# Optimization experiments

Hardware: AMD Instinct MI355X
Metric: run time of the kernel (lower is better)

Reference implementation:

```python
import jax, jax.numpy as jnp
import numpy as np

V = 6          # num_variables
K = 6          # codebook_size
D = 32         # embedding_dim
C = 3          # channels
B = 64         # batch
N = K ** V     # 46656 codebook combinations
EPS = 1e-5     # torch BatchNorm eps
ENTROPY_SCALE = 0.1


def setup_inputs() -> dict:
    key = jax.random.key(0)
    ks = jax.random.split(key, 40)
    i = iter(range(40))
    def rn(shape, s):
        return jax.random.normal(ks[next(i)], shape, dtype=jnp.float32) * s
    def rv(shape):
        return 0.5 + 0.5 * jax.random.uniform(ks[next(i)], shape, dtype=jnp.float32)
    inp = {
        'x': jax.random.normal(ks[next(i)], (B, C, 7, 7), dtype=jnp.float32),
        # encoder
        'conv_w': rn((256, C, 7, 7), 0.08), 'conv_b': rn((256,), 0.01),
        'ebn2_g': 1.0 + rn((256,), 0.1), 'ebn2_b': rn((256,), 0.1),
        'fc1_w': rn((1024, 256), 0.06), 'fc1_b': rn((1024,), 0.01),
        'ebn1_g': 1.0 + rn((1024,), 0.1), 'ebn1_b': rn((1024,), 0.1),
        'fc2_w': rn((V * K, 1024), 0.03), 'fc2_b': rn((V * K,), 0.01),
        # quantizer embeddings (V separate codebooks)
        'embeds': jax.random.normal(ks[next(i)], (V, K, D), dtype=jnp.float32),
        # decoder
        'dfc1_w': rn((1024, V * D), 0.07), 'dfc1_b': rn((1024,), 0.01),
        'dbn1_g': 1.0 + rn((1024,), 0.1), 'dbn1_b': rn((1024,), 0.1),
        'dbn1_rm': rn((1024,), 0.1), 'dbn1_rv': rv((1024,)),
        'dfc2_w': rn((256, 1024), 0.03), 'dfc2_b': rn((256,), 0.01),
        'dbn2_g': 1.0 + rn((256,), 0.1), 'dbn2_b': rn((256,), 0.1),
        'dbn2_rm': rn((256,), 0.1), 'dbn2_rv': rv((256,)),
        'dct1_w': rn((256, 16, 7, 7), 0.05), 'dct1_b': rn((16,), 0.01),
        'dbn3_g': 1.0 + rn((16,), 0.1), 'dbn3_b': rn((16,), 0.1),
        'dbn3_rm': rn((16,), 0.1), 'dbn3_rv': rv((16,)),
        'dct2_w': rn((16, C), 0.2), 'dct2_b': rn((C,), 0.01),
    }
    return inp


def _bn_eval(t, g, b, rm, rvar):
    # eval-mode BatchNorm (running stats); params broadcast over leading dims
    return g * (t - rm) * jax.lax.rsqrt(rvar + EPS) + b


def _bn_train(t, g, b):
    # train-mode BatchNorm1d on (B, F): biased batch statistics over dim 0
    m = t.mean(0)
    v = ((t - m) ** 2).mean(0)
    return g * (t - m) * jax.lax.rsqrt(v + EPS) + b


def _decode_all(embeds, dfc1_w, dfc1_b, dbn1_g, dbn1_b, dbn1_rm, dbn1_rv,
                dfc2_w, dfc2_b, dbn2_g, dbn2_b, dbn2_rm, dbn2_rv,
                dct1_w, dct1_b, dbn3_g, dbn3_b, dbn3_rm, dbn3_rv,
                dct2_w, dct2_b):
    # enumerate all K^V index tuples in itertools.product order (first var slowest)
    idx = jnp.arange(N)
    powers = K ** (V - 1 - jnp.arange(V))
    combos = (idx[:, None] // powers[None, :]) % K          # (N, V)
    z = embeds[jnp.arange(V)[None, :], combos]              # (N, V, D) gather
    h = z.reshape(N, V * D) @ dfc1_w.T + dfc1_b             # (N, 1024)
    h = jax.nn.relu(_bn_eval(h, dbn1_g, dbn1_b, dbn1_rm, dbn1_rv))
    h = h @ dfc2_w.T + dfc2_b                               # (N, 256)
    h = jax.nn.relu(_bn_eval(h, dbn2_g, dbn2_b, dbn2_rm, dbn2_rv))
    # ConvTranspose2d(256,16,7,stride=2) on 1x1 input == einsum with full kernel
    h = jnp.einsum('ni,iohw->nohw', h, dct1_w) + dct1_b[:, None, None]  # (N,16,7,7)
    h = jax.nn.relu(_bn_eval(h, dbn3_g[:, None, None], dbn3_b[:, None, None],
                             dbn3_rm[:, None, None], dbn3_rv[:, None, None]))
    # ConvTranspose2d(16,C,1,1) == pointwise channel mix
    em = jnp.einsum('nihw,io->nohw', h, dct2_w) + dct2_b[:, None, None]  # (N,C,7,7)
    return em


def reference(x, conv_w, conv_b, ebn2_g, ebn2_b, fc1_w, fc1_b, ebn1_g, ebn1_b,
              fc2_w, fc2_b, embeds, dfc1_w, dfc1_b, dbn1_g, dbn1_b, dbn1_rm,
              dbn1_rv, dfc2_w, dfc2_b, dbn2_g, dbn2_b, dbn2_rm, dbn2_rv,
              dct1_w, dct1_b, dbn3_g, dbn3_b, dbn3_rm, dbn3_rv, dct2_w, dct2_b):
    # emission means for every codebook combination (batched decode, BN eval)
    em = _decode_all(embeds, dfc1_w, dfc1_b, dbn1_g, dbn1_b, dbn1_rm, dbn1_rv,
                     dfc2_w, dfc2_b, dbn2_g, dbn2_b, dbn2_rm, dbn2_rv,
                     dct1_w, dct1_b, dbn3_g, dbn3_b, dbn3_rm, dbn3_rv,
                     dct2_w, dct2_b)                         # (N, C, 7, 7)
    # encoder: Conv2d(C,256,7) on 7x7 input collapses to a single GEMM
    e = jnp.einsum('bchw,ochw->bo', x, conv_w) + conv_b      # (B, 256)
    e = jax.nn.relu(_bn_train(e, ebn2_g, ebn2_b))
    e = e @ fc1_w.T + fc1_b                                  # (B, 1024)
    e = jax.nn.relu(_bn_train(e, ebn1_g, ebn1_b))
    logits = e @ fc2_w.T + fc2_b                             # (B, V*K)
    # quantizer
    latent_dist = jax.nn.softmax(logits.reshape(B, V, K), axis=-1)
    latent_loss = ENTROPY_SCALE * jnp.sum(
        latent_dist * jnp.log(latent_dist + 1e-10), axis=(1, 2))
    # obs logits: -0.5 * ||em - x||^2 summed over (C,H,W), via expanded form
    E = em.reshape(N, -1)                                    # (N, 147)
    X = x.reshape(B, -1)                                     # (B, 147)
    obs = -0.5 * (jnp.sum(E * E, -1)[None, :]
                  - 2.0 * (X @ E.T)
                  + jnp.sum(X * X, -1)[:, None])             # (B, N)
    obs_logits = obs.reshape((B,) + (K,) * V)
    return obs_logits, latent_dist, latent_loss
```

## Files before the change

### kernel.cpp

```cpp
#include <hip/hip_runtime.h>
#include <math.h>

#define EPSF 1e-5f
#define NNC 46656

typedef __attribute__((ext_vector_type(4))) float  f32x4;
typedef __attribute__((ext_vector_type(8))) short  short8;
typedef __attribute__((ext_vector_type(8))) unsigned short ushort8;
typedef __attribute__((ext_vector_type(4))) unsigned int uint4v;

__device__ __forceinline__ float bf2f(unsigned short u) {
    unsigned int x = ((unsigned int)u) << 16;
    return __builtin_bit_cast(float, x);
}
__device__ __forceinline__ unsigned short f2bf(float f) {
    unsigned int x = __builtin_bit_cast(unsigned int, f);
    unsigned int r = (x + 0x7fffu + ((x >> 16) & 1u)) >> 16;
    return (unsigned short)r;
}

#define WS_PP    0u
#define WS_C1    36864u
#define WS_SH    37888u
#define WS_S3    148480u
#define WS_W2BF  259072u
#define WS_C2    390144u
#define WS_W3BF  390400u
#define WS_C3    490752u
#define WS_XBF   490768u
#define WS_SX2   495888u
#define WS_E1T   495952u
#define WS_E2T   512336u

#define OBS_SIZE (64*NNC)
#define DIST_OFF OBS_SIZE
#define LOSS_OFF (OBS_SIZE + 64*36)

#define LDS_BYTES 77056


__global__ void dvae_k1(const float* __restrict__ x,
                        const float* __restrict__ conv_w, const float* __restrict__ conv_b,
                        const float* __restrict__ ebn2_g, const float* __restrict__ ebn2_b,
                        const float* __restrict__ embeds, const float* __restrict__ dfc1_w,
                        const float* __restrict__ dfc1_b,
                        const float* __restrict__ dbn1_g, const float* __restrict__ dbn1_b,
                        const float* __restrict__ dbn1_rm, const float* __restrict__ dbn1_rv,
                        const float* __restrict__ dfc2_w, const float* __restrict__ dfc2_b,
                        const float* __restrict__ dbn2_g, const float* __restrict__ dbn2_b,
                        const float* __restrict__ dbn2_rm, const float* __restrict__ dbn2_rv,
                        const float* __restrict__ dct1_w, const float* __restrict__ dct1_b,
                        const float* __restrict__ dbn3_g, const float* __restrict__ dbn3_b,
                        const float* __restrict__ dbn3_rm, const float* __restrict__ dbn3_rv,
                        float* __restrict__ ws) {
    __shared__ float wtile[64 * 193];
    __shared__ float semb[1152];
    int bx = blockIdx.x, tid = threadIdx.x;
    if (bx < 16) {
        int j0 = bx * 64;
        for (int e = tid; e < 64 * 192; e += 256)
            wtile[(e / 192) * 193 + (e % 192)] = dfc1_w[j0 * 192 + e];
        for (int e = tid; e < 1152; e += 256) semb[e] = embeds[e];
        __syncthreads();
        int jL = tid & 63, wvP = tid >> 6;
        int j = j0 + jL;
        float s1 = dbn1_g[j] * rsqrtf(dbn1_rv[j] + EPSF);
#pragma unroll
        for (int vkL = 0; vkL < 9; ++vkL) {
            int vk = wvP * 9 + vkL;
            int v = vk / 6;
            const float* wrow = &wtile[jL * 193 + v * 32];
            const float* ep = &semb[vk * 32];
            float dot = 0.f;
#pragma unroll
            for (int d = 0; d < 32; ++d) dot += wrow[d] * ep[d];
            ws[WS_PP + vk * 1024 + j] = s1 * dot;
        }
        if (tid < 64) {
            int jj = j0 + tid;
            float s = dbn1_g[jj] * rsqrtf(dbn1_rv[jj] + EPSF);
            ws[WS_C1 + jj] = s * dfc1_b[jj] + dbn1_b[jj] - dbn1_rm[jj] * s;
        }
    } else if (bx < 272) {
        int t = (bx - 16) * 256 + tid;
        int i = t >> 8, kq = (t & 255) * 4;
        float s2 = dbn2_g[i] * rsqrtf(dbn2_rv[i] + EPSF);
        float4 w = *(const float4*)(dfc2_w + i * 1024 + kq);
        unsigned short* dst = (unsigned short*)(ws + WS_W2BF) + i * 1024 + kq;
        dst[0] = f2bf(s2 * w.x); dst[1] = f2bf(s2 * w.y);
        dst[2] = f2bf(s2 * w.z); dst[3] = f2bf(s2 * w.w);
        if (kq == 0) ws[WS_C2 + i] = s2 * dfc2_b[i] + dbn2_b[i] - dbn2_rm[i] * s2;
    } else if (bx < 1056) {
        int t = (bx - 272) * 256 + tid;
        int up = t >> 8, k = t & 255;
        int o = up & 15, hw = up >> 4;
        float s3 = dbn3_g[o] * rsqrtf(dbn3_rv[o] + EPSF);
        ((unsigned short*)(ws + WS_W3BF))[t] = f2bf(s3 * dct1_w[k * 784 + o * 49 + hw]);
        if (t < 16) {
            float s = dbn3_g[t] * rsqrtf(dbn3_rv[t] + EPSF);
            ws[WS_C3 + t] = s * dct1_b[t] + dbn3_b[t] - dbn3_rm[t] * s;
        }
    } else if (bx == 1056) {
        unsigned short* Xb = (unsigned short*)(ws + WS_XBF);
        if (tid < 64) {
            const float* xp = x + tid * 147;
            float s = 0.f;
            for (int qq = 0; qq < 147; ++qq) { float v = xp[qq]; s += v * v; }
            ws[WS_SX2 + tid] = s;
        }
        for (int e = tid; e < 64 * 160; e += 256) {
            int b = e / 160, col = e % 160;
            float v = 0.f;
            if (col < 147) { int hw = col / 3, c = col % 3; v = x[b * 147 + c * 49 + hw]; }
            Xb[e] = f2bf(v);
        }
    } else {
        int blk = bx - 1057;
        int b = tid & 63, oL = tid >> 6;
        int o = blk * 4 + oL;
        const float* xp = x + b * 147;
        const float* wp = conv_w + o * 147;
        float acc = conv_b[o];
        for (int qq = 0; qq < 147; ++qq) acc += xp[qq] * wp[qq];
        float m = acc;
#pragma unroll
        for (int s = 1; s < 64; s <<= 1) m += __shfl_xor(m, s);
        m *= (1.f / 64.f);
        float d = acc - m;
        float var = d * d;
#pragma unroll
        for (int s = 1; s < 64; s <<= 1) var += __shfl_xor(var, s);
        var *= (1.f / 64.f);
        float y = ebn2_g[o] * d * rsqrtf(var + EPSF) + ebn2_b[o];
        ws[WS_E1T + o * 64 + b] = fmaxf(y, 0.f);
    }
}


__global__ void dvae_k2(const float* __restrict__ fc1_w, const float* __restrict__ fc1_b,
                        const float* __restrict__ ebn1_g, const float* __restrict__ ebn1_b,
                        float* __restrict__ ws) {
    int bx = blockIdx.x, tid = threadIdx.x;
    const float* Pp = ws + WS_PP;
    if (bx < 108) {
        int t = bx * 256 + tid;
        int gh = t >> 7, kg = (t & 127) * 8;
        int d0 = gh / 36, d1 = (gh / 6) % 6, d2 = gh % 6;
        const float* r0 = Pp + d0 * 1024 + kg;
        const float* r1 = Pp + (6 + d1) * 1024 + kg;
        const float* r2 = Pp + (12 + d2) * 1024 + kg;
        const float* cc = ws + WS_C1 + kg;
        ushort8 o;
#pragma unroll
        for (int e = 0; e < 8; ++e) o[e] = f2bf(cc[e] + r0[e] + r1[e] + r2[e]);
        *(ushort8*)((unsigned short*)(ws + WS_SH) + gh * 1024 + kg) = o;
    } else if (bx < 216) {
        int t = (bx - 108) * 256 + tid;
        int gl = t >> 7, kg = (t & 127) * 8;
        int d3 = gl / 36, d4 = (gl / 6) % 6, d5 = gl % 6;
        const float* r3 = Pp + (18 + d3) * 1024 + kg;
        const float* r4 = Pp + (24 + d4) * 1024 + kg;
        const float* r5 = Pp + (30 + d5) * 1024 + kg;
        ushort8 o;
#pragma unroll
        for (int e = 0; e < 8; ++e) o[e] = f2bf(r3[e] + r4[e] + r5[e]);
        *(ushort8*)((unsigned short*)(ws + WS_S3) + gl * 1024 + kg) = o;
    } else {
        int blk = bx - 216;
        int b = tid & 63, jL = tid >> 6;
        int j = blk * 4 + jL;
        const float* e1 = ws + WS_E1T;
        const float* wp = fc1_w + j * 256;
        float acc = fc1_b[j];
        for (int o = 0; o < 256; ++o) acc += e1[o * 64 + b] * wp[o];
        float m = acc;
#pragma unroll
        for (int s = 1; s < 64; s <<= 1) m += __shfl_xor(m, s);
        m *= (1.f / 64.f);
        float d = acc - m;
        float var = d * d;
#pragma unroll
        for (int s = 1; s < 64; s <<= 1) var += __shfl_xor(var, s);
        var *= (1.f / 64.f);
        float y = ebn1_g[j] * d * rsqrtf(var + EPSF) + ebn1_b[j];
        ws[WS_E2T + j * 64 + b] = fmaxf(y, 0.f);
    }
}


__launch_bounds__(256, 2)
__global__ void dvae_k3(const unsigned short* __restrict__ Sh,
                        const unsigned short* __restrict__ S3g,
                        const unsigned short* __restrict__ W2,
                        const float* __restrict__ c2g,
                        const unsigned short* __restrict__ W3,
                        const float* __restrict__ c3g,
                        const float* __restrict__ d2wg,
                        const float* __restrict__ d2bg,
                        const unsigned short* __restrict__ Xg,
                        const float* __restrict__ sx2g,
                        const float* __restrict__ e2T,
                        const float* __restrict__ fc2_w,
                        const float* __restrict__ fc2_b,
                        float* __restrict__ out) {
    extern __shared__ char sm[];
    int tid = threadIdx.x;

    if (blockIdx.x == 0) {
        float* wch = (float*)sm;
        float* ech = (float*)(sm + 18432);
        float* LG  = (float*)(sm + 51200);
        int b = tid & 63;
        int wvU = __builtin_amdgcn_readfirstlane(tid >> 6);
        float accv[9];
#pragma unroll
        for (int it = 0; it < 9; ++it) accv[it] = 0.f;
        for (int ch = 0; ch < 8; ++ch) {
            __syncthreads();
            for (int e = tid; e < 36 * 128; e += 256) {
                int o = e >> 7, jl = e & 127;
                wch[e] = fc2_w[o * 1024 + ch * 128 + jl];
            }
            for (int e = tid; e < 128 * 64; e += 256)
                ech[e] = e2T[(ch * 128 + (e >> 6)) * 64 + (e & 63)];
            __syncthreads();
            for (int jl = 0; jl < 128; ++jl) {
                float ev = ech[jl * 64 + b];
#pragma unroll
                for (int it = 0; it < 9; ++it)
                    accv[it] += ev * wch[(wvU + it * 4) * 128 + jl];
            }
        }
#pragma unroll
        for (int it = 0; it < 9; ++it) {
            int o = wvU + it * 4;
            LG[b * 36 + o] = accv[it] + fc2_b[o];
        }
        __syncthreads();
        if (tid < 64) {
            float loss = 0.f;
#pragma unroll
            for (int v = 0; v < 6; ++v) {
                float mx = -1e30f;
#pragma unroll
                for (int k = 0; k < 6; ++k) mx = fmaxf(mx, LG[tid * 36 + v * 6 + k]);
                float s = 0.f, ex[6];
#pragma unroll
                for (int k = 0; k < 6; ++k) { ex[k] = expf(LG[tid * 36 + v * 6 + k] - mx); s += ex[k]; }
                float inv = 1.f / s;
#pragma unroll
                for (int k = 0; k < 6; ++k) {
                    float dd = ex[k] * inv;
                    out[DIST_OFF + tid * 36 + v * 6 + k] = dd;
                    loss += dd * logf(dd + 1e-10f);
                }
            }
            out[LOSS_OFF + tid] = 0.1f * loss;
        }
        return;
    }

    int wv = tid >> 6, lane = tid & 63, l15 = lane & 15, q = lane >> 4;
    int nbase = (blockIdx.x - 1) * 64;
    float* sE2p = (float*)(sm + 0);
    float* sE2f = (float*)(sm + 1024);
    unsigned short* Albs = (unsigned short*)(sm + 1280);
    unsigned short* emL  = (unsigned short*)(sm + 1280);
    float* h3w = (wv < 2) ? (float*)(sm + 21760 + wv * 5120)
                          : (float*)(sm + 34048 + (wv - 2) * 5120);
    unsigned short* h2L = (unsigned short*)(sm + 44288);
    unsigned short* XL  = (unsigned short*)(sm + 44288);

    f32x4 acc[4][4];
#pragma unroll
    for (int a = 0; a < 4; ++a)
#pragma unroll
        for (int b = 0; b < 4; ++b) acc[a][b] = (f32x4){0.f, 0.f, 0.f, 0.f};

    int mB = tid >> 2, sub = tid & 3;
    int nm = nbase + mB;
    int gh = nm / 216;
    int r216 = nm - gh * 216;
    const unsigned short* shp = Sh + gh * 1024 + sub * 64;
    const unsigned short* s3p = S3g + r216 * 1024 + sub * 64;

    for (int kc = 0; kc < 4; ++kc) {
        __syncthreads();
        int kb = kc * 256;
        ushort8 hv8[8], sv8[8];
#pragma unroll
        for (int t = 0; t < 8; ++t) {
            hv8[t] = *(const ushort8*)(shp + kb + t * 8);
            sv8[t] = *(const ushort8*)(s3p + kb + t * 8);
        }
#pragma unroll
        for (int t = 0; t < 8; ++t) {
            uint4v H = __builtin_bit_cast(uint4v, hv8[t]);
            uint4v S = __builtin_bit_cast(uint4v, sv8[t]);
            uint4v O;
#pragma unroll
            for (int d = 0; d < 4; ++d) {
                float hlo = __builtin_bit_cast(float, H[d] << 16);
                float hhi = __builtin_bit_cast(float, H[d] & 0xffff0000u);
                float slo = __builtin_bit_cast(float, S[d] << 16);
                float shi = __builtin_bit_cast(float, S[d] & 0xffff0000u);
                unsigned int rlo = __builtin_bit_cast(unsigned int, fmaxf(hlo + slo, 0.f));
                unsigned int rhi = __builtin_bit_cast(unsigned int, fmaxf(hhi + shi, 0.f));
                O[d] = (rlo >> 16) | (rhi & 0xffff0000u);
            }
            *(ushort8*)(Albs + ((sub * 8 + t) * 64 + mB) * 8) = __builtin_bit_cast(ushort8, O);
        }
        __syncthreads();
        const unsigned short* bbase = W2 + (wv * 64 + l15) * 1024 + kb + q * 8;
        short8 bpre[4];
#pragma unroll
        for (int j = 0; j < 4; ++j) bpre[j] = *(const short8*)(bbase + j * 16384);
#pragma unroll
        for (int s = 0; s < 8; ++s) {
            short8 bcur[4];
#pragma unroll
            for (int j = 0; j < 4; ++j) bcur[j] = bpre[j];
            if (s < 7) {
#pragma unroll
                for (int j = 0; j < 4; ++j)
                    bpre[j] = *(const short8*)(bbase + j * 16384 + (s + 1) * 32);
            }
            short8 af[4];
#pragma unroll
            for (int mt = 0; mt < 4; ++mt)
                af[mt] = *(const short8*)(Albs + ((s * 4 + q) * 64 + mt * 16 + l15) * 8);
#pragma unroll
            for (int mt = 0; mt < 4; ++mt)
#pragma unroll
                for (int j = 0; j < 4; ++j)
                    acc[mt][j] = __builtin_amdgcn_mfma_f32_16x16x32_bf16(af[mt], bcur[j], acc[mt][j], 0, 0, 0);
        }
    }
#pragma unroll
    for (int j = 0; j < 4; ++j) {
        int i = wv * 64 + j * 16 + l15;
        float cc = c2g[i];
#pragma unroll
        for (int mt = 0; mt < 4; ++mt)
#pragma unroll
            for (int r = 0; r < 4; ++r) {
                int m = mt * 16 + q * 4 + r;
                h2L[((i >> 3) * 64 + m) * 8 + (i & 7)] = f2bf(fmaxf(acc[mt][j][r] + cc, 0.f));
            }
    }
    __syncthreads();

    float c3v = c3g[l15];
    float db0 = d2bg[0], db1 = d2bg[1], db2 = d2bg[2];
    float dw0[16], dw1[16], dw2[16];
#pragma unroll
    for (int o = 0; o < 16; ++o) {
        dw0[o] = d2wg[o * 3 + 0]; dw1[o] = d2wg[o * 3 + 1]; dw2[o] = d2wg[o * 3 + 2];
    }
    float sE2a = 0.f;
    for (int c = wv; c < 13; c += 4) {
        int hw0 = c * 4;
        f32x4 a2[4][4];
#pragma unroll
        for (int a = 0; a < 4; ++a)
#pragma unroll
            for (int b = 0; b < 4; ++b) a2[a][b] = (f32x4){0.f, 0.f, 0.f, 0.f};
        const unsigned short* b3[4];
#pragma unroll
        for (int j = 0; j < 4; ++j) {
            int hw = hw0 + j; if (hw > 48) hw = 48;
            b3[j] = W3 + (hw * 16 + l15) * 256 + q * 8;
        }
        short8 bpre[4];
#pragma unroll
        for (int j = 0; j < 4; ++j) bpre[j] = *(const short8*)(b3[j]);
#pragma unroll
        for (int s = 0; s < 8; ++s) {
            short8 bcur[4];
#pragma unroll
            for (int j = 0; j < 4; ++j) bcur[j] = bpre[j];
            if (s < 7) {
#pragma unroll
                for (int j = 0; j < 4; ++j) bpre[j] = *(const short8*)(b3[j] + (s + 1) * 32);
            }
            short8 af[4];
#pragma unroll
            for (int mt = 0; mt < 4; ++mt)
                af[mt] = *(const short8*)(h2L + ((s * 4 + q) * 64 + mt * 16 + l15) * 8);
#pragma unroll
            for (int mt = 0; mt < 4; ++mt)
#pragma unroll
                for (int j = 0; j < 4; ++j)
                    a2[mt][j] = __builtin_amdgcn_mfma_f32_16x16x32_bf16(af[mt], bcur[j], a2[mt][j], 0, 0, 0);
        }
#pragma unroll
        for (int j = 0; j < 4; ++j) {
            int hw = hw0 + j;
            if (hw <= 48) {
#pragma unroll
                for (int mt = 0; mt < 4; ++mt)
#pragma unroll
                    for (int r = 0; r < 4; ++r)
                        h3w[(mt * 16 + q * 4 + r) * 20 + l15] = fmaxf(a2[mt][j][r] + c3v, 0.f);
                float hvv[16];
#pragma unroll
                for (int g = 0; g < 4; ++g) {
                    f32x4 tv = *(const f32x4*)(h3w + lane * 20 + g * 4);
                    hvv[g * 4 + 0] = tv[0]; hvv[g * 4 + 1] = tv[1];
                    hvv[g * 4 + 2] = tv[2]; hvv[g * 4 + 3] = tv[3];
                }
                float e0 = db0, e1 = db1, e2 = db2;
#pragma unroll
                for (int o = 0; o < 16; ++o) {
                    e0 += hvv[o] * dw0[o]; e1 += hvv[o] * dw1[o]; e2 += hvv[o] * dw2[o];
                }
                unsigned short u0 = f2bf(e0), u1 = f2bf(e1), u2 = f2bf(e2);
                float f0 = bf2f(u0), f1 = bf2f(u1), f2v = bf2f(u2);
                sE2a += f0 * f0 + f1 * f1 + f2v * f2v;
                emL[lane * 160 + hw * 3 + 0] = u0;
                emL[lane * 160 + hw * 3 + 1] = u1;
                emL[lane * 160 + hw * 3 + 2] = u2;
            }
        }
    }
    sE2p[wv * 64 + lane] = sE2a;
    __syncthreads();

    if (tid < 64) sE2f[tid] = sE2p[tid] + sE2p[64 + tid] + sE2p[128 + tid] + sE2p[192 + tid];
    for (int e = tid; e < 64 * 13; e += 256) emL[(e / 13) * 160 + 147 + (e % 13)] = 0;
    for (int e = tid; e < 1280; e += 256)
        *(ushort8*)(XL + e * 8) = *(const ushort8*)(Xg + e * 8);
    __syncthreads();

    f32x4 aO[4];
#pragma unroll
    for (int j = 0; j < 4; ++j) aO[j] = (f32x4){0.f, 0.f, 0.f, 0.f};
    const unsigned short* xrow = XL + (wv * 16 + l15) * 160 + q * 8;
#pragma unroll
    for (int s = 0; s < 5; ++s) {
        short8 af = *(const short8*)(xrow + s * 32);
#pragma unroll
        for (int j = 0; j < 4; ++j) {
            short8 bfv = *(const short8*)(emL + (j * 16 + l15) * 160 + s * 32 + q * 8);
            aO[j] = __builtin_amdgcn_mfma_f32_16x16x32_bf16(af, bfv, aO[j], 0, 0, 0);
        }
    }
    int b0 = wv * 16 + q * 4;
    float sxv[4];
#pragma unroll
    for (int r = 0; r < 4; ++r) sxv[r] = sx2g[b0 + r];
#pragma unroll
    for (int j = 0; j < 4; ++j) {
        int n = nbase + j * 16 + l15;
        float he = 0.5f * sE2f[j * 16 + l15];
#pragma unroll
        for (int r = 0; r < 4; ++r)
            out[(size_t)(b0 + r) * NNC + n] = aO[j][r] - he - 0.5f * sxv[r];
    }
}


extern "C" void kernel_launch(void* const* d_in, const int* in_sizes, int n_in,
                              void* d_out, int out_size, void* d_ws, size_t ws_size,
                              hipStream_t stream) {
    const float* x       = (const float*)d_in[0];
    const float* conv_w  = (const float*)d_in[1];
    const float* conv_b  = (const float*)d_in[2];
    const float* ebn2_g  = (const float*)d_in[3];
    const float* ebn2_b  = (const float*)d_in[4];
    const float* fc1_w   = (const float*)d_in[5];
    const float* fc1_b   = (const float*)d_in[6];
    const float* ebn1_g  = (const float*)d_in[7];
    const float* ebn1_b  = (const float*)d_in[8];
    const float* fc2_w   = (const float*)d_in[9];
    const float* fc2_b   = (const float*)d_in[10];
    const float* embeds  = (const float*)d_in[11];
    const float* dfc1_w  = (const float*)d_in[12];
    const float* dfc1_b  = (const float*)d_in[13];
    const float* dbn1_g  = (const float*)d_in[14];
    const float* dbn1_b  = (const float*)d_in[15];
    const float* dbn1_rm = (const float*)d_in[16];
    const float* dbn1_rv = (const float*)d_in[17];
    const float* dfc2_w  = (const float*)d_in[18];
    const float* dfc2_b  = (const float*)d_in[19];
    const float* dbn2_g  = (const float*)d_in[20];
    const float* dbn2_b  = (const float*)d_in[21];
    const float* dbn2_rm = (const float*)d_in[22];
    const float* dbn2_rv = (const float*)d_in[23];
    const float* dct1_w  = (const float*)d_in[24];
    const float* dct1_b  = (const float*)d_in[25];
    const float* dbn3_g  = (const float*)d_in[26];
    const float* dbn3_b  = (const float*)d_in[27];
    const float* dbn3_rm = (const float*)d_in[28];
    const float* dbn3_rv = (const float*)d_in[29];
    const float* dct2_w  = (const float*)d_in[30];
    const float* dct2_b  = (const float*)d_in[31];

    float* ws  = (float*)d_ws;
    float* out = (float*)d_out;

    dvae_k1<<<1121, 256, 0, stream>>>(x, conv_w, conv_b, ebn2_g, ebn2_b,
                                      embeds, dfc1_w, dfc1_b, dbn1_g, dbn1_b, dbn1_rm, dbn1_rv,
                                      dfc2_w, dfc2_b, dbn2_g, dbn2_b, dbn2_rm, dbn2_rv,
                                      dct1_w, dct1_b, dbn3_g, dbn3_b, dbn3_rm, dbn3_rv, ws);
    dvae_k2<<<472, 256, 0, stream>>>(fc1_w, fc1_b, ebn1_g, ebn1_b, ws);

    hipFuncSetAttribute(reinterpret_cast<const void*>(dvae_k3),
                        hipFuncAttributeMaxDynamicSharedMemorySize, LDS_BYTES);
    dvae_k3<<<730, 256, LDS_BYTES, stream>>>(
        (const unsigned short*)(ws + WS_SH), (const unsigned short*)(ws + WS_S3),
        (const unsigned short*)(ws + WS_W2BF), ws + WS_C2,
        (const unsigned short*)(ws + WS_W3BF), ws + WS_C3,
        dct2_w, dct2_b,
        (const unsigned short*)(ws + WS_XBF), ws + WS_SX2,
        ws + WS_E2T, fc2_w, fc2_b, out);
}
```

Baseline: 281.2 us.

## Stream GEMM A-operands from global registers, restage dct1 transpose and conv input via LDS

In the main decode kernel, the relu(Sh+S3) A-operand is no longer staged through LDS with barriers per K-chunk. Each lane now loads its MFMA fragments straight from global memory and packs them in registers, with a one-step prefetch over 32 K-steps, which frees LDS and removes syncs. The X operand for the obs GEMM is read directly from global memory instead of being copied into LDS. In the prep kernel, the dct1 weight transpose is done through an LDS tile with vectorised bf16 stores, cutting the block count from 1121 to 353, and the conv stage caches x in LDS. readfirstlane hints mark the wave-uniform row indices. The trade-off is more global and L2 traffic from redundant fragment reads and higher register pressure.

```diff
diff --git a/kernel.cpp b/kernel.cpp
--- a/kernel.cpp
+++ b/kernel.cpp
@@ -17,6 +17,23 @@
     unsigned int x = __builtin_bit_cast(unsigned int, f);
     unsigned int r = (x + 0x7fffu + ((x >> 16) & 1u)) >> 16;
     return (unsigned short)r;
+}
+
+__device__ __forceinline__ short8 packrelu8(ushort8 H8, ushort8 S8) {
+    uint4v H = __builtin_bit_cast(uint4v, H8);
+    uint4v S = __builtin_bit_cast(uint4v, S8);
+    uint4v O;
+#pragma unroll
+    for (int d = 0; d < 4; ++d) {
+        float hlo = __builtin_bit_cast(float, H[d] << 16);
+        float hhi = __builtin_bit_cast(float, H[d] & 0xffff0000u);
+        float slo = __builtin_bit_cast(float, S[d] << 16);
+        float shi = __builtin_bit_cast(float, S[d] & 0xffff0000u);
+        unsigned int rlo = __builtin_bit_cast(unsigned int, fmaxf(hlo + slo, 0.f));
+        unsigned int rhi = __builtin_bit_cast(unsigned int, fmaxf(hhi + shi, 0.f));
+        O[d] = __builtin_amdgcn_perm(rhi, rlo, 0x07060302u);
+    }
+    return __builtin_bit_cast(short8, O);
 }
 
 #define WS_PP    0u
@@ -36,7 +53,7 @@
 #define DIST_OFF OBS_SIZE
 #define LOSS_OFF (OBS_SIZE + 64*36)
 
-#define LDS_BYTES 77056
+#define LDS_BYTES 75008
 
 
 __global__ void dvae_k1(const float* __restrict__ x,
@@ -53,10 +70,11 @@
                         const float* __restrict__ dbn3_g, const float* __restrict__ dbn3_b,
                         const float* __restrict__ dbn3_rm, const float* __restrict__ dbn3_rv,
                         float* __restrict__ ws) {
-    __shared__ float wtile[64 * 193];
-    __shared__ float semb[1152];
+    __shared__ float sbuf[13504];
     int bx = blockIdx.x, tid = threadIdx.x;
     if (bx < 16) {
+        float* wtile = sbuf;
+        float* semb  = sbuf + 12352;
         int j0 = bx * 64;
         for (int e = tid; e < 64 * 192; e += 256)
             wtile[(e / 192) * 193 + (e % 192)] = dfc1_w[j0 * 192 + e];
@@ -90,17 +108,26 @@
         dst[0] = f2bf(s2 * w.x); dst[1] = f2bf(s2 * w.y);
         dst[2] = f2bf(s2 * w.z); dst[3] = f2bf(s2 * w.w);
         if (kq == 0) ws[WS_C2 + i] = s2 * dfc2_b[i] + dbn2_b[i] - dbn2_rm[i] * s2;
-    } else if (bx < 1056) {
-        int t = (bx - 272) * 256 + tid;
-        int up = t >> 8, k = t & 255;
-        int o = up & 15, hw = up >> 4;
-        float s3 = dbn3_g[o] * rsqrtf(dbn3_rv[o] + EPSF);
-        ((unsigned short*)(ws + WS_W3BF))[t] = f2bf(s3 * dct1_w[k * 784 + o * 49 + hw]);
-        if (t < 16) {
-            float s = dbn3_g[t] * rsqrtf(dbn3_rv[t] + EPSF);
-            ws[WS_C3 + t] = s * dct1_b[t] + dbn3_b[t] - dbn3_rm[t] * s;
-        }
-    } else if (bx == 1056) {
+    } else if (bx < 288) {
+        int blk = bx - 272;
+        for (int e = tid; e < 12544; e += 256) sbuf[e] = dct1_w[blk * 12544 + e];
+        __syncthreads();
+        unsigned short* W3 = (unsigned short*)(ws + WS_W3BF);
+        for (int e = tid; e < 1568; e += 256) {
+            int up = e >> 1, k8 = (e & 1) * 8;
+            int o = up & 15, hw = up >> 4;
+            float s3 = dbn3_g[o] * rsqrtf(dbn3_rv[o] + EPSF);
+            ushort8 ov;
+#pragma unroll
+            for (int t = 0; t < 8; ++t)
+                ov[t] = f2bf(s3 * sbuf[(k8 + t) * 784 + o * 49 + hw]);
+            *(ushort8*)(W3 + up * 256 + blk * 16 + k8) = ov;
+        }
+        if (blk == 0 && tid < 16) {
+            float s = dbn3_g[tid] * rsqrtf(dbn3_rv[tid] + EPSF);
+            ws[WS_C3 + tid] = s * dct1_b[tid] + dbn3_b[tid] - dbn3_rm[tid] * s;
+        }
+    } else if (bx == 288) {
         unsigned short* Xb = (unsigned short*)(ws + WS_XBF);
         if (tid < 64) {
             const float* xp = x + tid * 147;
@@ -115,13 +142,15 @@
             Xb[e] = f2bf(v);
         }
     } else {
-        int blk = bx - 1057;
-        int b = tid & 63, oL = tid >> 6;
+        int blk = bx - 289;
+        for (int e = tid; e < 9408; e += 256) sbuf[e] = x[e];
+        __syncthreads();
+        int b = tid & 63;
+        int oL = __builtin_amdgcn_readfirstlane(tid >> 6);
         int o = blk * 4 + oL;
-        const float* xp = x + b * 147;
         const float* wp = conv_w + o * 147;
         float acc = conv_b[o];
-        for (int qq = 0; qq < 147; ++qq) acc += xp[qq] * wp[qq];
+        for (int qq = 0; qq < 147; ++qq) acc += sbuf[b * 147 + qq] * wp[qq];
         float m = acc;
 #pragma unroll
         for (int s = 1; s < 64; s <<= 1) m += __shfl_xor(m, s);
@@ -167,7 +196,8 @@
         *(ushort8*)((unsigned short*)(ws + WS_S3) + gl * 1024 + kg) = o;
     } else {
         int blk = bx - 216;
-        int b = tid & 63, jL = tid >> 6;
+        int b = tid & 63;
+        int jL = __builtin_amdgcn_readfirstlane(tid >> 6);
         int j = blk * 4 + jL;
         const float* e1 = ws + WS_E1T;
         const float* wp = fc1_w + j * 256;
@@ -264,12 +294,9 @@
     int nbase = (blockIdx.x - 1) * 64;
     float* sE2p = (float*)(sm + 0);
     float* sE2f = (float*)(sm + 1024);
-    unsigned short* Albs = (unsigned short*)(sm + 1280);
-    unsigned short* emL  = (unsigned short*)(sm + 1280);
-    float* h3w = (wv < 2) ? (float*)(sm + 21760 + wv * 5120)
-                          : (float*)(sm + 34048 + (wv - 2) * 5120);
-    unsigned short* h2L = (unsigned short*)(sm + 44288);
-    unsigned short* XL  = (unsigned short*)(sm + 44288);
+    unsigned short* emL = (unsigned short*)(sm + 1280);
+    float* h3w = (float*)(sm + 21760 + wv * 5120);
+    unsigned short* h2L = (unsigned short*)(sm + 42240);
 
     f32x4 acc[4][4];
 #pragma unroll
@@ -277,64 +304,48 @@
 #pragma unroll
         for (int b = 0; b < 4; ++b) acc[a][b] = (f32x4){0.f, 0.f, 0.f, 0.f};
 
-    int mB = tid >> 2, sub = tid & 3;
-    int nm = nbase + mB;
-    int gh = nm / 216;
-    int r216 = nm - gh * 216;
-    const unsigned short* shp = Sh + gh * 1024 + sub * 64;
-    const unsigned short* s3p = S3g + r216 * 1024 + sub * 64;
-
-    for (int kc = 0; kc < 4; ++kc) {
-        __syncthreads();
-        int kb = kc * 256;
-        ushort8 hv8[8], sv8[8];
-#pragma unroll
-        for (int t = 0; t < 8; ++t) {
-            hv8[t] = *(const ushort8*)(shp + kb + t * 8);
-            sv8[t] = *(const ushort8*)(s3p + kb + t * 8);
-        }
-#pragma unroll
-        for (int t = 0; t < 8; ++t) {
-            uint4v H = __builtin_bit_cast(uint4v, hv8[t]);
-            uint4v S = __builtin_bit_cast(uint4v, sv8[t]);
-            uint4v O;
-#pragma unroll
-            for (int d = 0; d < 4; ++d) {
-                float hlo = __builtin_bit_cast(float, H[d] << 16);
-                float hhi = __builtin_bit_cast(float, H[d] & 0xffff0000u);
-                float slo = __builtin_bit_cast(float, S[d] << 16);
-                float shi = __builtin_bit_cast(float, S[d] & 0xffff0000u);
-                unsigned int rlo = __builtin_bit_cast(unsigned int, fmaxf(hlo + slo, 0.f));
-                unsigned int rhi = __builtin_bit_cast(unsigned int, fmaxf(hhi + shi, 0.f));
-                O[d] = (rlo >> 16) | (rhi & 0xffff0000u);
-            }
-            *(ushort8*)(Albs + ((sub * 8 + t) * 64 + mB) * 8) = __builtin_bit_cast(ushort8, O);
-        }
-        __syncthreads();
-        const unsigned short* bbase = W2 + (wv * 64 + l15) * 1024 + kb + q * 8;
-        short8 bpre[4];
-#pragma unroll
-        for (int j = 0; j < 4; ++j) bpre[j] = *(const short8*)(bbase + j * 16384);
-#pragma unroll
-        for (int s = 0; s < 8; ++s) {
-            short8 bcur[4];
-#pragma unroll
-            for (int j = 0; j < 4; ++j) bcur[j] = bpre[j];
-            if (s < 7) {
-#pragma unroll
-                for (int j = 0; j < 4; ++j)
-                    bpre[j] = *(const short8*)(bbase + j * 16384 + (s + 1) * 32);
-            }
-            short8 af[4];
-#pragma unroll
-            for (int mt = 0; mt < 4; ++mt)
-                af[mt] = *(const short8*)(Albs + ((s * 4 + q) * 64 + mt * 16 + l15) * 8);
-#pragma unroll
-            for (int mt = 0; mt < 4; ++mt)
-#pragma unroll
-                for (int j = 0; j < 4; ++j)
-                    acc[mt][j] = __builtin_amdgcn_mfma_f32_16x16x32_bf16(af[mt], bcur[j], acc[mt][j], 0, 0, 0);
-        }
+    const unsigned short* pSh[4];
+    const unsigned short* pS3[4];
+#pragma unroll
+    for (int mt = 0; mt < 4; ++mt) {
+        int nm = nbase + mt * 16 + l15;
+        int gh = nm / 216;
+        int r216 = nm - gh * 216;
+        pSh[mt] = Sh + gh * 1024 + q * 8;
+        pS3[mt] = S3g + r216 * 1024 + q * 8;
+    }
+    const unsigned short* bbase = W2 + (wv * 64 + l15) * 1024 + q * 8;
+
+    ushort8 sa[4], sb[4];
+    short8 bpre[4];
+#pragma unroll
+    for (int mt = 0; mt < 4; ++mt) { sa[mt] = *(const ushort8*)(pSh[mt]); sb[mt] = *(const ushort8*)(pS3[mt]); }
+#pragma unroll
+    for (int j = 0; j < 4; ++j) bpre[j] = *(const short8*)(bbase + j * 16384);
+
+#pragma unroll 2
+    for (int s = 0; s < 32; ++s) {
+        short8 af[4];
+#pragma unroll
+        for (int mt = 0; mt < 4; ++mt) af[mt] = packrelu8(sa[mt], sb[mt]);
+        short8 bcur[4];
+#pragma unroll
+        for (int j = 0; j < 4; ++j) bcur[j] = bpre[j];
+        if (s < 31) {
+            int off = (s + 1) * 32;
+#pragma unroll
+            for (int mt = 0; mt < 4; ++mt) {
+                sa[mt] = *(const ushort8*)(pSh[mt] + off);
+                sb[mt] = *(const ushort8*)(pS3[mt] + off);
+            }
+#pragma unroll
+            for (int j = 0; j < 4; ++j) bpre[j] = *(const short8*)(bbase + j * 16384 + off);
+        }
+#pragma unroll
+        for (int mt = 0; mt < 4; ++mt)
+#pragma unroll
+            for (int j = 0; j < 4; ++j)
+                acc[mt][j] = __builtin_amdgcn_mfma_f32_16x16x32_bf16(af[mt], bcur[j], acc[mt][j], 0, 0, 0);
     }
 #pragma unroll
     for (int j = 0; j < 4; ++j) {
@@ -371,17 +382,17 @@
             int hw = hw0 + j; if (hw > 48) hw = 48;
             b3[j] = W3 + (hw * 16 + l15) * 256 + q * 8;
         }
-        short8 bpre[4];
-#pragma unroll
-        for (int j = 0; j < 4; ++j) bpre[j] = *(const short8*)(b3[j]);
+        short8 bpre2[4];
+#pragma unroll
+        for (int j = 0; j < 4; ++j) bpre2[j] = *(const short8*)(b3[j]);
 #pragma unroll
         for (int s = 0; s < 8; ++s) {
             short8 bcur[4];
 #pragma unroll
-            for (int j = 0; j < 4; ++j) bcur[j] = bpre[j];
+            for (int j = 0; j < 4; ++j) bcur[j] = bpre2[j];
             if (s < 7) {
 #pragma unroll
-                for (int j = 0; j < 4; ++j) bpre[j] = *(const short8*)(b3[j] + (s + 1) * 32);
+                for (int j = 0; j < 4; ++j) bpre2[j] = *(const short8*)(b3[j] + (s + 1) * 32);
             }
             short8 af[4];
 #pragma unroll
@@ -424,18 +435,15 @@
         }
     }
     sE2p[wv * 64 + lane] = sE2a;
+    for (int e = tid; e < 64 * 13; e += 256) emL[(e / 13) * 160 + 147 + (e % 13)] = 0;
     __syncthreads();
-
     if (tid < 64) sE2f[tid] = sE2p[tid] + sE2p[64 + tid] + sE2p[128 + tid] + sE2p[192 + tid];
-    for (int e = tid; e < 64 * 13; e += 256) emL[(e / 13) * 160 + 147 + (e % 13)] = 0;
-    for (int e = tid; e < 1280; e += 256)
-        *(ushort8*)(XL + e * 8) = *(const ushort8*)(Xg + e * 8);
     __syncthreads();
 
     f32x4 aO[4];
 #pragma unroll
     for (int j = 0; j < 4; ++j) aO[j] = (f32x4){0.f, 0.f, 0.f, 0.f};
-    const unsigned short* xrow = XL + (wv * 16 + l15) * 160 + q * 8;
+    const unsigned short* xrow = Xg + (wv * 16 + l15) * 160 + q * 8;
 #pragma unroll
     for (int s = 0; s < 5; ++s) {
         short8 af = *(const short8*)(xrow + s * 32);
@@ -499,10 +507,10 @@
     float* ws  = (float*)d_ws;
     float* out = (float*)d_out;
 
-    dvae_k1<<<1121, 256, 0, stream>>>(x, conv_w, conv_b, ebn2_g, ebn2_b,
-                                      embeds, dfc1_w, dfc1_b, dbn1_g, dbn1_b, dbn1_rm, dbn1_rv,
-                                      dfc2_w, dfc2_b, dbn2_g, dbn2_b, dbn2_rm, dbn2_rv,
-                                      dct1_w, dct1_b, dbn3_g, dbn3_b, dbn3_rm, dbn3_rv, ws);
+    dvae_k1<<<353, 256, 0, stream>>>(x, conv_w, conv_b, ebn2_g, ebn2_b,
+                                     embeds, dfc1_w, dfc1_b, dbn1_g, dbn1_b, dbn1_rm, dbn1_rv,
+                                     dfc2_w, dfc2_b, dbn2_g, dbn2_b, dbn2_rm, dbn2_rv,
+                                     dct1_w, dct1_b, dbn3_g, dbn3_b, dbn3_rm, dbn3_rv, ws);
     dvae_k2<<<472, 256, 0, stream>>>(fc1_w, fc1_b, ebn1_g, ebn1_b, ws);
 
     hipFuncSetAttribute(reinterpret_cast<const void*>(dvae_k3),
```

Measured after the change: 279.1 us. About the same (-0.7%).
